# Optimization experiments

Hardware: AMD Instinct MI355X
Metric: run time of the kernel (lower is better)

Reference implementation:

```python
import jax, jax.numpy as jnp
import numpy as np

B, T, D = 32, 2048, 128


def setup_inputs() -> dict:
    key = jax.random.key(0)
    k1, k2, k3 = jax.random.split(key, 3)
    values = jax.random.normal(k1, (B, T, D), dtype=jnp.float32)
    # monotonically increasing per-feature timestamps (irregular sampling)
    times = jnp.cumsum(jax.random.uniform(k2, (B, T, D), dtype=jnp.float32), axis=1)
    mask = jax.random.randint(k3, (B, T, D), 0, 2) > 0  # True = observed
    return {"values": values, "times": times, "mask": mask}


def _fill(x, t, mask):
    """Parallel forward fill (LOCF) and backward fill (NOCB) of x and t.

    Replaces the serial Keras RNN scan with cummax/cummin over observation
    indices followed by a gather. Matches ForwardCell semantics:
      forward : x init 0, t init times[:, 0, :]
      backward: x init 0, t init max(times, axis=1)
    """
    Tn = x.shape[1]
    ar = jnp.broadcast_to(jnp.arange(Tn, dtype=jnp.int32)[None, :, None], x.shape)
    # ---- forward fill ----
    fidx = jax.lax.cummax(jnp.where(mask, ar, -1), axis=1)  # last observed idx
    fvalid = fidx >= 0
    fi = jnp.clip(fidx, 0, Tn - 1)
    x_last = jnp.where(fvalid, jnp.take_along_axis(x, fi, axis=1), 0.0)
    t_last = jnp.where(fvalid, jnp.take_along_axis(t, fi, axis=1), t[:, :1, :])
    # ---- backward fill ----
    bidx = jax.lax.cummin(jnp.where(mask, ar, Tn), axis=1, reverse=True)  # next observed idx
    bvalid = bidx < Tn
    bi = jnp.clip(bidx, 0, Tn - 1)
    x_next = jnp.where(bvalid, jnp.take_along_axis(x, bi, axis=1), 0.0)
    t_next = jnp.where(bvalid, jnp.take_along_axis(t, bi, axis=1),
                       jnp.max(t, axis=1, keepdims=True))
    return x_last, t_last, x_next, t_next


def reference(values, times, mask):
    x_last, t_last, x_next, t_next = _fill(values, times, mask)
    denom = t_next - t_last
    num = x_last * (t_next - times) + x_next * (times - t_last)
    safe = denom != 0.0
    x_itp = num / jnp.where(safe, denom, 1.0)
    x_itp = jnp.where(safe & jnp.isfinite(x_itp), x_itp, 0.0)  # nan/inf -> 0
    return jnp.where(mask, values, x_itp)
```

## Files before the change

kernel.cpp:

```cpp
#include <hip/hip_runtime.h>
#include <math.h>

constexpr int B  = 32;
constexpr int T  = 2048;
constexpr int D  = 128;
constexpr int C  = 16;
constexpr int NC = T / C;

__global__ __launch_bounds__(256)
void linterp_kernel(const float* __restrict__ values,
                    const float* __restrict__ times,
                    const int*   __restrict__ mask,
                    float*       __restrict__ out)
{
    const int gid   = blockIdx.x * 256 + threadIdx.x;
    const int d     = gid & (D - 1);
    const int chunk = (gid >> 7) & (NC - 1);
    const int b     = gid >> 14;

    const int seq_base = b * T * D + d;
    const int t0i      = chunk * C;

    float v[C], tm[C];
    unsigned int mbits = 0;
#pragma unroll
    for (int i = 0; i < C; ++i) {
        const int off = seq_base + (t0i + i) * D;
        v[i]  = values[off];
        tm[i] = times[off];
        mbits |= (mask[off] != 0 ? 1u : 0u) << i;
    }

    const float t_first = times[seq_base];
    const float t_lastT = times[seq_base + (T - 1) * D];

    float fx = 0.f, ft = t_first;
    if (chunk > 0) {
        unsigned int pb = 0;
#pragma unroll
        for (int i = 0; i < C; ++i) {
            const int off = seq_base + (t0i - C + i) * D;
            pb |= (mask[off] != 0 ? 1u : 0u) << i;
        }
        if (pb != 0u) {
            const int idx = 31 - __builtin_clz(pb);
            const int off = seq_base + (t0i - C + idx) * D;
            fx = values[off]; ft = times[off];
        } else {
            for (int j = t0i - C - 1; j >= 0; --j) {
                const int off = seq_base + j * D;
                if (mask[off] != 0) { fx = values[off]; ft = times[off]; break; }
            }
        }
    }

    float bx = 0.f, bt = t_lastT;
    if (chunk < NC - 1) {
        unsigned int nb = 0;
#pragma unroll
        for (int i = 0; i < C; ++i) {
            const int off = seq_base + (t0i + C + i) * D;
            nb |= (mask[off] != 0 ? 1u : 0u) << i;
        }
        if (nb != 0u) {
            const int idx = __builtin_ctz(nb);
            const int off = seq_base + (t0i + C + idx) * D;
            bx = values[off]; bt = times[off];
        } else {
            for (int j = t0i + 2 * C; j < T; ++j) {
                const int off = seq_base + j * D;
                if (mask[off] != 0) { bx = values[off]; bt = times[off]; break; }
            }
        }
    }

    float xl[C], tl[C];
#pragma unroll
    for (int i = 0; i < C; ++i) {
        if ((mbits >> i) & 1u) { fx = v[i]; ft = tm[i]; }
        xl[i] = fx;
        tl[i] = ft;
    }

#pragma unroll
    for (int i = C - 1; i >= 0; --i) {
        const bool obs = (mbits >> i) & 1u;
        if (obs) { bx = v[i]; bt = tm[i]; }
        const float denom = bt - tl[i];
        const float num   = xl[i] * (bt - tm[i]) + bx * (tm[i] - tl[i]);
        const bool  safe  = (denom != 0.f);
        float xi = num / (safe ? denom : 1.f);
        xi = (safe && isfinite(xi)) ? xi : 0.f;
        out[seq_base + (t0i + i) * D] = obs ? v[i] : xi;
    }
}

extern "C" void kernel_launch(void* const* d_in, const int* in_sizes, int n_in,
                              void* d_out, int out_size, void* d_ws, size_t ws_size,
                              hipStream_t stream)
{
    const float* values = (const float*)d_in[0];
    const float* times  = (const float*)d_in[1];
    const int*   mask   = (const int*)d_in[2];
    float*       out    = (float*)d_out;

    const int total_threads = B * NC * D;
    linterp_kernel<<<total_threads / 256, 256, 0, stream>>>(values, times, mask, out);
}
```

Baseline: 134.0 us.

## Pack mask into bitwords and vectorize interpolation with float4 tiles

Adds a pre-pass kernel that compresses the int32 mask into 32-bit words per feature, stored in workspace. A new interpolation kernel processes 4x4 tiles with float4 loads and stores and finds the previous and next observation with clz/ctz on the packed words. This cuts mask reads and the redundant neighbour-chunk rescans of the old kernel. The cost is an extra kernel launch and a workspace round-trip, with the old kernel kept as a fallback when no workspace is given.

```diff
diff --git a/kernel.cpp b/kernel.cpp
--- a/kernel.cpp
+++ b/kernel.cpp
@@ -4,8 +4,152 @@
 constexpr int B  = 32;
 constexpr int T  = 2048;
 constexpr int D  = 128;
+constexpr int NW = T / 32;
 constexpr int C  = 16;
 constexpr int NC = T / C;
+
+__global__ __launch_bounds__(256)
+void pack_mask_kernel(const int* __restrict__ mask, unsigned* __restrict__ packed)
+{
+    const int gid = blockIdx.x * 256 + threadIdx.x;
+    const int d4 = gid & 31;
+    const int w  = (gid >> 5) & (NW - 1);
+    const int b  = gid >> 11;
+
+    const int4* m4 = reinterpret_cast<const int4*>(mask)
+                   + (((size_t)(b * T + (w << 5)) * D) >> 2) + d4;
+    unsigned r0 = 0, r1 = 0, r2 = 0, r3 = 0;
+#pragma unroll
+    for (int i = 0; i < 32; ++i) {
+        const int4 m = m4[i * (D >> 2)];
+        r0 |= (m.x != 0 ? 1u : 0u) << i;
+        r1 |= (m.y != 0 ? 1u : 0u) << i;
+        r2 |= (m.z != 0 ? 1u : 0u) << i;
+        r3 |= (m.w != 0 ? 1u : 0u) << i;
+    }
+    uint4 o; o.x = r0; o.y = r1; o.z = r2; o.w = r3;
+    reinterpret_cast<uint4*>(packed + (size_t)(b * NW + w) * D)[d4] = o;
+}
+
+__global__ __launch_bounds__(256)
+void interp4_kernel(const float* __restrict__ values,
+                    const float* __restrict__ times,
+                    const unsigned* __restrict__ packed,
+                    float* __restrict__ out)
+{
+    const int gid = blockIdx.x * 256 + threadIdx.x;
+    const int d4 = gid & 31;
+    const int c  = (gid >> 5) & 511;
+    const int b  = gid >> 14;
+    const int d0 = d4 << 2;
+    const int t0 = c << 2;
+    const int tw = t0 >> 5;
+    const int sh = t0 & 31;
+
+    const size_t bbase = (size_t)b * T * D;
+    const float* vrow = values + bbase + (size_t)t0 * D + d0;
+    const float* trow = times  + bbase + (size_t)t0 * D + d0;
+
+    float vv[4][4], tt[4][4];
+#pragma unroll
+    for (int i = 0; i < 4; ++i) {
+        const float4 a = *reinterpret_cast<const float4*>(vrow + i * D);
+        const float4 s = *reinterpret_cast<const float4*>(trow + i * D);
+        vv[i][0] = a.x; vv[i][1] = a.y; vv[i][2] = a.z; vv[i][3] = a.w;
+        tt[i][0] = s.x; tt[i][1] = s.y; tt[i][2] = s.z; tt[i][3] = s.w;
+    }
+
+    const unsigned* pk = packed + (size_t)b * NW * D;
+    const uint4 pw    = *reinterpret_cast<const uint4*>(pk + (size_t)tw * D + d0);
+    const uint4 pprev = (tw > 0)
+        ? *reinterpret_cast<const uint4*>(pk + (size_t)(tw - 1) * D + d0) : make_uint4(0,0,0,0);
+    const uint4 pnext = (tw < NW - 1)
+        ? *reinterpret_cast<const uint4*>(pk + (size_t)(tw + 1) * D + d0) : make_uint4(0,0,0,0);
+
+    const float4 tf4 = *reinterpret_cast<const float4*>(times + bbase + d0);
+    const float4 tl4 = *reinterpret_cast<const float4*>(times + bbase + (size_t)(T - 1) * D + d0);
+    const float tfirst[4] = {tf4.x, tf4.y, tf4.z, tf4.w};
+    const float tlastT[4] = {tl4.x, tl4.y, tl4.z, tl4.w};
+
+    const unsigned pwj[4] = {pw.x, pw.y, pw.z, pw.w};
+    const unsigned ppj[4] = {pprev.x, pprev.y, pprev.z, pprev.w};
+    const unsigned pnj[4] = {pnext.x, pnext.y, pnext.z, pnext.w};
+
+    int fi[4], bi[4];
+#pragma unroll
+    for (int j = 0; j < 4; ++j) {
+        const unsigned wlow = sh ? (pwj[j] & ((1u << sh) - 1u)) : 0u;
+        int f = -1;
+        if (wlow)        f = (tw << 5) + 31 - __builtin_clz(wlow);
+        else if (ppj[j]) f = ((tw - 1) << 5) + 31 - __builtin_clz(ppj[j]);
+        else {
+            for (int ww = tw - 2; ww >= 0; --ww) {
+                const unsigned x = pk[(size_t)ww * D + d0 + j];
+                if (x) { f = (ww << 5) + 31 - __builtin_clz(x); break; }
+            }
+        }
+        fi[j] = f;
+
+        const int eh = sh + 4;
+        const unsigned whigh = (eh < 32) ? (pwj[j] >> eh) : 0u;
+        int n = -1;
+        if (whigh)       n = (tw << 5) + eh + __builtin_ctz(whigh);
+        else if (pnj[j]) n = ((tw + 1) << 5) + __builtin_ctz(pnj[j]);
+        else {
+            for (int ww = tw + 2; ww < NW; ++ww) {
+                const unsigned x = pk[(size_t)ww * D + d0 + j];
+                if (x) { n = (ww << 5) + __builtin_ctz(x); break; }
+            }
+        }
+        bi[j] = n;
+    }
+
+    float fx[4], ft[4], bx[4], bt[4];
+#pragma unroll
+    for (int j = 0; j < 4; ++j) {
+        const size_t offF = bbase + (size_t)(fi[j] < 0 ? 0 : fi[j]) * D + d0 + j;
+        const size_t offB = bbase + (size_t)(bi[j] < 0 ? 0 : bi[j]) * D + d0 + j;
+        fx[j] = values[offF]; ft[j] = times[offF];
+        bx[j] = values[offB]; bt[j] = times[offB];
+    }
+#pragma unroll
+    for (int j = 0; j < 4; ++j) {
+        if (fi[j] < 0) { fx[j] = 0.f; ft[j] = tfirst[j]; }
+        if (bi[j] < 0) { bx[j] = 0.f; bt[j] = tlastT[j]; }
+    }
+
+    float res[4][4];
+#pragma unroll
+    for (int j = 0; j < 4; ++j) {
+        const unsigned mb = (pwj[j] >> sh) & 0xFu;
+        float xl[4], tl[4];
+        float cfx = fx[j], cft = ft[j];
+#pragma unroll
+        for (int i = 0; i < 4; ++i) {
+            if ((mb >> i) & 1u) { cfx = vv[i][j]; cft = tt[i][j]; }
+            xl[i] = cfx; tl[i] = cft;
+        }
+        float cbx = bx[j], cbt = bt[j];
+#pragma unroll
+        for (int i = 3; i >= 0; --i) {
+            const bool obs = (mb >> i) & 1u;
+            if (obs) { cbx = vv[i][j]; cbt = tt[i][j]; }
+            const float denom = cbt - tl[i];
+            const float num   = xl[i] * (cbt - tt[i][j]) + cbx * (tt[i][j] - tl[i]);
+            const bool  safe  = (denom != 0.f);
+            float xi = num / (safe ? denom : 1.f);
+            xi = (safe && isfinite(xi)) ? xi : 0.f;
+            res[i][j] = obs ? vv[i][j] : xi;
+        }
+    }
+
+    float* orow = out + bbase + (size_t)t0 * D + d0;
+#pragma unroll
+    for (int i = 0; i < 4; ++i) {
+        float4 o; o.x = res[i][0]; o.y = res[i][1]; o.z = res[i][2]; o.w = res[i][3];
+        *reinterpret_cast<float4*>(orow + i * D) = o;
+    }
+}
 
 __global__ __launch_bounds__(256)
 void linterp_kernel(const float* __restrict__ values,
@@ -54,7 +198,7 @@
         }
     }
 
-    float bx = 0.f, bt = t_lastT;
+    float bxv = 0.f, btv = t_lastT;
     if (chunk < NC - 1) {
         unsigned int nb = 0;
 #pragma unroll
@@ -65,11 +209,11 @@
         if (nb != 0u) {
             const int idx = __builtin_ctz(nb);
             const int off = seq_base + (t0i + C + idx) * D;
-            bx = values[off]; bt = times[off];
+            bxv = values[off]; btv = times[off];
         } else {
             for (int j = t0i + 2 * C; j < T; ++j) {
                 const int off = seq_base + j * D;
-                if (mask[off] != 0) { bx = values[off]; bt = times[off]; break; }
+                if (mask[off] != 0) { bxv = values[off]; btv = times[off]; break; }
             }
         }
     }
@@ -85,9 +229,9 @@
 #pragma unroll
     for (int i = C - 1; i >= 0; --i) {
         const bool obs = (mbits >> i) & 1u;
-        if (obs) { bx = v[i]; bt = tm[i]; }
-        const float denom = bt - tl[i];
-        const float num   = xl[i] * (bt - tm[i]) + bx * (tm[i] - tl[i]);
+        if (obs) { bxv = v[i]; btv = tm[i]; }
+        const float denom = btv - tl[i];
+        const float num   = xl[i] * (btv - tm[i]) + bxv * (tm[i] - tl[i]);
         const bool  safe  = (denom != 0.f);
         float xi = num / (safe ? denom : 1.f);
         xi = (safe && isfinite(xi)) ? xi : 0.f;
@@ -104,6 +248,12 @@
     const int*   mask   = (const int*)d_in[2];
     float*       out    = (float*)d_out;
 
-    const int total_threads = B * NC * D;
-    linterp_kernel<<<total_threads / 256, 256, 0, stream>>>(values, times, mask, out);
-}
+    const size_t PACKED_BYTES = (size_t)B * NW * D * sizeof(unsigned);
+    if (d_ws != nullptr && ws_size >= PACKED_BYTES) {
+        unsigned* packed = (unsigned*)d_ws;
+        pack_mask_kernel<<<(B * NW * (D / 4)) / 256, 256, 0, stream>>>(mask, packed);
+        interp4_kernel<<<(B * (T / 4) * (D / 4)) / 256, 256, 0, stream>>>(values, times, packed, out);
+    } else {
+        linterp_kernel<<<(B * NC * D) / 256, 256, 0, stream>>>(values, times, mask, out);
+    }
+}
```

After: 143.1 us. +6.8%, slower.

## Use float4 vectorized 4x4 tiles per thread with neighbor mask window scans

Applied to the files above, without the earlier changes.

Each thread now handles a 4-timestep by 4-feature tile, loading values, times and mask with 128-bit vector loads and writing results with float4 stores. It finds neighboring observations by scanning 16 mask rows before and after the tile, also vectorized, and falls back to a scalar search only when that window has none. This reduces the number of memory instructions and widens transactions compared with the scalar per-thread 16-step chunks. The cost is heavier redundant mask traffic: each 4-row tile reads 32 extra neighbor rows of mask, versus 32 extra rows per 16-row chunk before.

```diff
diff --git a/kernel.cpp b/kernel.cpp
--- a/kernel.cpp
+++ b/kernel.cpp
@@ -1,97 +1,140 @@
 #include <hip/hip_runtime.h>
 #include <math.h>
 
-constexpr int B  = 32;
-constexpr int T  = 2048;
-constexpr int D  = 128;
-constexpr int C  = 16;
-constexpr int NC = T / C;
+constexpr int B = 32;
+constexpr int T = 2048;
+constexpr int D = 128;
 
 __global__ __launch_bounds__(256)
-void linterp_kernel(const float* __restrict__ values,
-                    const float* __restrict__ times,
-                    const int*   __restrict__ mask,
-                    float*       __restrict__ out)
+void interp_wide_kernel(const float* __restrict__ values,
+                        const float* __restrict__ times,
+                        const int*   __restrict__ mask,
+                        float*       __restrict__ out)
 {
-    const int gid   = blockIdx.x * 256 + threadIdx.x;
-    const int d     = gid & (D - 1);
-    const int chunk = (gid >> 7) & (NC - 1);
-    const int b     = gid >> 14;
+    const int gid = blockIdx.x * 256 + threadIdx.x;
+    const int d4 = gid & 31;
+    const int c  = (gid >> 5) & 511;
+    const int b  = gid >> 14;
+    const int d0 = d4 << 2;
+    const int t0 = c << 2;
 
-    const int seq_base = b * T * D + d;
-    const int t0i      = chunk * C;
+    const size_t bbase = (size_t)b * T * D;
+    const float* vrow = values + bbase + (size_t)t0 * D + d0;
+    const float* trow = times  + bbase + (size_t)t0 * D + d0;
+    const int*   mrow = mask   + bbase + (size_t)t0 * D + d0;
 
-    float v[C], tm[C];
-    unsigned int mbits = 0;
+    float vv[4][4], tt[4][4];
+    unsigned mb[4] = {0u, 0u, 0u, 0u};
 #pragma unroll
-    for (int i = 0; i < C; ++i) {
-        const int off = seq_base + (t0i + i) * D;
-        v[i]  = values[off];
-        tm[i] = times[off];
-        mbits |= (mask[off] != 0 ? 1u : 0u) << i;
+    for (int i = 0; i < 4; ++i) {
+        const float4 a = *reinterpret_cast<const float4*>(vrow + i * D);
+        const float4 s = *reinterpret_cast<const float4*>(trow + i * D);
+        const int4   m = *reinterpret_cast<const int4*>(mrow + i * D);
+        vv[i][0] = a.x; vv[i][1] = a.y; vv[i][2] = a.z; vv[i][3] = a.w;
+        tt[i][0] = s.x; tt[i][1] = s.y; tt[i][2] = s.z; tt[i][3] = s.w;
+        mb[0] |= (m.x != 0 ? 1u : 0u) << i;
+        mb[1] |= (m.y != 0 ? 1u : 0u) << i;
+        mb[2] |= (m.z != 0 ? 1u : 0u) << i;
+        mb[3] |= (m.w != 0 ? 1u : 0u) << i;
     }
 
-    const float t_first = times[seq_base];
-    const float t_lastT = times[seq_base + (T - 1) * D];
+    unsigned fw[4] = {0u, 0u, 0u, 0u};
+    unsigned bw[4] = {0u, 0u, 0u, 0u};
+#pragma unroll
+    for (int k = 0; k < 16; ++k) {
+        const int st = t0 - 16 + k;
+        if (st >= 0) {
+            const int4 m = *reinterpret_cast<const int4*>(
+                mask + bbase + (size_t)st * D + d0);
+            fw[0] |= (m.x != 0 ? 1u : 0u) << k;
+            fw[1] |= (m.y != 0 ? 1u : 0u) << k;
+            fw[2] |= (m.z != 0 ? 1u : 0u) << k;
+            fw[3] |= (m.w != 0 ? 1u : 0u) << k;
+        }
+    }
+#pragma unroll
+    for (int k = 0; k < 16; ++k) {
+        const int st = t0 + 4 + k;
+        if (st < T) {
+            const int4 m = *reinterpret_cast<const int4*>(
+                mask + bbase + (size_t)st * D + d0);
+            bw[0] |= (m.x != 0 ? 1u : 0u) << k;
+            bw[1] |= (m.y != 0 ? 1u : 0u) << k;
+            bw[2] |= (m.z != 0 ? 1u : 0u) << k;
+            bw[3] |= (m.w != 0 ? 1u : 0u) << k;
+        }
+    }
 
-    float fx = 0.f, ft = t_first;
-    if (chunk > 0) {
-        unsigned int pb = 0;
+    int fi[4], bi[4];
 #pragma unroll
-        for (int i = 0; i < C; ++i) {
-            const int off = seq_base + (t0i - C + i) * D;
-            pb |= (mask[off] != 0 ? 1u : 0u) << i;
+    for (int j = 0; j < 4; ++j) {
+        fi[j] = fw[j] ? (t0 - 16 + (31 - __builtin_clz(fw[j]))) : -1;
+        bi[j] = bw[j] ? (t0 + 4 + __builtin_ctz(bw[j])) : -1;
+    }
+#pragma unroll
+    for (int j = 0; j < 4; ++j) {
+        if (fi[j] < 0 && t0 > 16) {
+            for (int st = t0 - 17; st >= 0; --st) {
+                if (mask[bbase + (size_t)st * D + d0 + j] != 0) { fi[j] = st; break; }
+            }
         }
-        if (pb != 0u) {
-            const int idx = 31 - __builtin_clz(pb);
-            const int off = seq_base + (t0i - C + idx) * D;
-            fx = values[off]; ft = times[off];
-        } else {
-            for (int j = t0i - C - 1; j >= 0; --j) {
-                const int off = seq_base + j * D;
-                if (mask[off] != 0) { fx = values[off]; ft = times[off]; break; }
+        if (bi[j] < 0 && t0 + 20 < T) {
+            for (int st = t0 + 20; st < T; ++st) {
+                if (mask[bbase + (size_t)st * D + d0 + j] != 0) { bi[j] = st; break; }
             }
         }
     }
 
-    float bx = 0.f, bt = t_lastT;
-    if (chunk < NC - 1) {
-        unsigned int nb = 0;
+    float fx[4], ft[4], bx[4], bt[4];
 #pragma unroll
-        for (int i = 0; i < C; ++i) {
-            const int off = seq_base + (t0i + C + i) * D;
-            nb |= (mask[off] != 0 ? 1u : 0u) << i;
+    for (int j = 0; j < 4; ++j) {
+        const int sF = fi[j] < 0 ? 0 : fi[j];
+        const int sB = bi[j] < 0 ? 0 : bi[j];
+        const size_t oF = bbase + (size_t)sF * D + d0 + j;
+        const size_t oB = bbase + (size_t)sB * D + d0 + j;
+        fx[j] = values[oF]; ft[j] = times[oF];
+        bx[j] = values[oB]; bt[j] = times[oB];
+    }
+    const float4 tf4 = *reinterpret_cast<const float4*>(times + bbase + d0);
+    const float4 tl4 = *reinterpret_cast<const float4*>(
+        times + bbase + (size_t)(T - 1) * D + d0);
+    const float tfirst[4] = {tf4.x, tf4.y, tf4.z, tf4.w};
+    const float tlastT[4] = {tl4.x, tl4.y, tl4.z, tl4.w};
+#pragma unroll
+    for (int j = 0; j < 4; ++j) {
+        if (fi[j] < 0) { fx[j] = 0.f; ft[j] = tfirst[j]; }
+        if (bi[j] < 0) { bx[j] = 0.f; bt[j] = tlastT[j]; }
+    }
+
+    float res[4][4];
+#pragma unroll
+    for (int j = 0; j < 4; ++j) {
+        float xl[4], tl[4];
+        float cfx = fx[j], cft = ft[j];
+#pragma unroll
+        for (int i = 0; i < 4; ++i) {
+            if ((mb[j] >> i) & 1u) { cfx = vv[i][j]; cft = tt[i][j]; }
+            xl[i] = cfx; tl[i] = cft;
         }
-        if (nb != 0u) {
-            const int idx = __builtin_ctz(nb);
-            const int off = seq_base + (t0i + C + idx) * D;
-            bx = values[off]; bt = times[off];
-        } else {
-            for (int j = t0i + 2 * C; j < T; ++j) {
-                const int off = seq_base + j * D;
-                if (mask[off] != 0) { bx = values[off]; bt = times[off]; break; }
-            }
+        float cbx = bx[j], cbt = bt[j];
+#pragma unroll
+        for (int i = 3; i >= 0; --i) {
+            const bool obs = (mb[j] >> i) & 1u;
+            if (obs) { cbx = vv[i][j]; cbt = tt[i][j]; }
+            const float denom = cbt - tl[i];
+            const float num   = xl[i] * (cbt - tt[i][j]) + cbx * (tt[i][j] - tl[i]);
+            const bool  safe  = (denom != 0.f);
+            float xi = num / (safe ? denom : 1.f);
+            xi = (safe && isfinite(xi)) ? xi : 0.f;
+            res[i][j] = obs ? vv[i][j] : xi;
         }
     }
 
-    float xl[C], tl[C];
+    float* orow = out + bbase + (size_t)t0 * D + d0;
 #pragma unroll
-    for (int i = 0; i < C; ++i) {
-        if ((mbits >> i) & 1u) { fx = v[i]; ft = tm[i]; }
-        xl[i] = fx;
-        tl[i] = ft;
-    }
-
-#pragma unroll
-    for (int i = C - 1; i >= 0; --i) {
-        const bool obs = (mbits >> i) & 1u;
-        if (obs) { bx = v[i]; bt = tm[i]; }
-        const float denom = bt - tl[i];
-        const float num   = xl[i] * (bt - tm[i]) + bx * (tm[i] - tl[i]);
-        const bool  safe  = (denom != 0.f);
-        float xi = num / (safe ? denom : 1.f);
-        xi = (safe && isfinite(xi)) ? xi : 0.f;
-        out[seq_base + (t0i + i) * D] = obs ? v[i] : xi;
+    for (int i = 0; i < 4; ++i) {
+        float4 o; o.x = res[i][0]; o.y = res[i][1]; o.z = res[i][2]; o.w = res[i][3];
+        *reinterpret_cast<float4*>(orow + i * D) = o;
     }
 }
 
@@ -104,6 +147,6 @@
     const int*   mask   = (const int*)d_in[2];
     float*       out    = (float*)d_out;
 
-    const int total_threads = B * NC * D;
-    linterp_kernel<<<total_threads / 256, 256, 0, stream>>>(values, times, mask, out);
+    const int total_threads = B * (T / 4) * (D / 4);
+    interp_wide_kernel<<<total_threads / 256, 256, 0, stream>>>(values, times, mask, out);
 }
```

After: 161.3 us. 1.2x slower.
